# Kernel tuning notes

Measured on AMD Instinct MI355X. Metric: run time of the kernel, lower is better.

Reference implementation:

```python
import jax, jax.numpy as jnp
import numpy as np

B, H, W, C = 32, 56, 56, 512
WS, SHIFT, NH = 7, 3, 16
N = WS * WS
NW = (H // WS) * (W // WS)
HID = 4 * C
EPS = 1e-5


def _np_constants():
    # log-spaced relative coords table (SwinV2 CPB input), pretrained_window_size=[0,0]
    rh = np.arange(-(WS - 1), WS, dtype=np.float32)
    tbl = np.stack(np.meshgrid(rh, rh, indexing='ij'), axis=-1)  # (2*WS-1, 2*WS-1, 2)
    tbl = tbl / (WS - 1) * 8.0
    tbl = np.sign(tbl) * np.log2(np.abs(tbl) + 1.0) / np.log2(8.0)
    coords = np.stack(np.meshgrid(np.arange(WS), np.arange(WS), indexing='ij'))
    cf = coords.reshape(2, -1)
    rc = (cf[:, :, None] - cf[:, None, :]).transpose(1, 2, 0).copy()  # (N,N,2)
    rc[..., 0] += WS - 1
    rc[..., 1] += WS - 1
    rc[..., 0] *= 2 * WS - 1
    rpi = rc.sum(-1)  # (N,N) indices into the (2*WS-1)^2 table
    # shifted-window attention mask
    img = np.zeros((H, W), dtype=np.float32)
    sl = (slice(0, -WS), slice(-WS, -SHIFT), slice(-SHIFT, None))
    cnt = 0
    for hs in sl:
        for ws in sl:
            img[hs, ws] = cnt
            cnt += 1
    mw = img.reshape(H // WS, WS, W // WS, WS).transpose(0, 2, 1, 3).reshape(-1, N)
    am = mw[:, None, :] - mw[:, :, None]
    attn_mask = np.where(am != 0, -100.0, 0.0).astype(np.float32)  # (NW,N,N)
    return tbl.reshape(-1, 2).astype(np.float32), rpi.reshape(-1), attn_mask

TBL_NP, RPI_NP, MASK_NP = _np_constants()


def _ln(x, g, b):
    mu = jnp.mean(x, -1, keepdims=True)
    var = jnp.mean((x - mu) ** 2, -1, keepdims=True)
    return (x - mu) * jax.lax.rsqrt(var + EPS) * g + b


def _win_part(x):  # (B,H,W,C) -> (B*NW, N, C)
    x = x.reshape(B, H // WS, WS, W // WS, WS, C).transpose(0, 1, 3, 2, 4, 5)
    return x.reshape(-1, N, C)


def _win_rev(w):  # (B*NW, N, C) -> (B,H,W,C)
    x = w.reshape(B, H // WS, W // WS, WS, WS, C).transpose(0, 1, 3, 2, 4, 5)
    return x.reshape(B, H, W, C)


def setup_inputs() -> dict:
    key = jax.random.key(0)
    ks = jax.random.split(key, 8)
    s = 0.02
    return {
        'x': jax.random.normal(ks[0], (B, H * W, C), jnp.float32),
        'qkv_w': jax.random.normal(ks[1], (3 * C, C), jnp.float32) * s,
        'q_bias': jnp.zeros((C,), jnp.float32),
        'v_bias': jnp.zeros((C,), jnp.float32),
        'logit_scale': jnp.log(10.0) * jnp.ones((NH, 1, 1), jnp.float32),
        'cpb_w1': jax.random.normal(ks[2], (512, 2), jnp.float32) * s,
        'cpb_b1': jnp.zeros((512,), jnp.float32),
        'cpb_w2': jax.random.normal(ks[3], (NH, 512), jnp.float32) * s,
        'proj_w': jax.random.normal(ks[4], (C, C), jnp.float32) * s,
        'proj_b': jnp.zeros((C,), jnp.float32),
        'norm1_g': jnp.ones((C,), jnp.float32),
        'norm1_b': jnp.zeros((C,), jnp.float32),
        'fc1_w': jax.random.normal(ks[5], (HID, C), jnp.float32) * s,
        'fc1_b': jnp.zeros((HID,), jnp.float32),
        'fc2_w': jax.random.normal(ks[6], (C, HID), jnp.float32) * s,
        'fc2_b': jnp.zeros((C,), jnp.float32),
        'norm2_g': jnp.ones((C,), jnp.float32),
        'norm2_b': jnp.zeros((C,), jnp.float32),
    }


def reference(x, qkv_w, q_bias, v_bias, logit_scale, cpb_w1, cpb_b1, cpb_w2,
              proj_w, proj_b, norm1_g, norm1_b, fc1_w, fc1_b, fc2_w, fc2_b,
              norm2_g, norm2_b):
    tbl = jnp.asarray(TBL_NP)
    mask = jnp.asarray(MASK_NP)
    shortcut = x
    xi = x.reshape(B, H, W, C)
    xi = jnp.roll(xi, shift=(-SHIFT, -SHIFT), axis=(1, 2))
    xw = _win_part(xi)  # (B*NW, N, C)
    qkv_bias = jnp.concatenate([q_bias, jnp.zeros_like(v_bias), v_bias])
    qkv = xw @ qkv_w.T + qkv_bias
    qkv = qkv.reshape(-1, N, 3, NH, C // NH).transpose(2, 0, 3, 1, 4)
    q, k, v = qkv[0], qkv[1], qkv[2]  # (B_, NH, N, hd)
    qn = q / jnp.maximum(jnp.linalg.norm(q, axis=-1, keepdims=True), 1e-12)
    kn = k / jnp.maximum(jnp.linalg.norm(k, axis=-1, keepdims=True), 1e-12)
    scale = jnp.exp(jnp.minimum(logit_scale, jnp.log(100.0)))  # (NH,1,1)
    attn = jnp.einsum('bhnd,bhmd->bhnm', qn, kn) * scale
    # CPB MLP -> relative position bias
    hcb = jax.nn.relu(tbl @ cpb_w1.T + cpb_b1)       # (169, 512)
    bias_tbl = hcb @ cpb_w2.T                        # (169, NH)
    rpb = bias_tbl[RPI_NP].reshape(N, N, NH).transpose(2, 0, 1)
    rpb = 16.0 * jax.nn.sigmoid(rpb)
    attn = attn + rpb[None]
    attn = attn.reshape(B, NW, NH, N, N) + mask[None, :, None]
    attn = jax.nn.softmax(attn.reshape(-1, NH, N, N), axis=-1)
    out = jnp.einsum('bhnm,bhmd->bhnd', attn, v).transpose(0, 2, 1, 3).reshape(-1, N, C)
    out = out @ proj_w.T + proj_b
    xi = _win_rev(out)
    xi = jnp.roll(xi, shift=(SHIFT, SHIFT), axis=(1, 2)).reshape(B, H * W, C)
    x = shortcut + _ln(xi, norm1_g, norm1_b)  # SwinV2 post-norm residual
    hmlp = jax.nn.gelu(x @ fc1_w.T + fc1_b, approximate=False)
    m = hmlp @ fc2_w.T + fc2_b
    x = x + _ln(m, norm2_g, norm2_b)
    return x
```

## Files before the change

### kernel.cpp

```cpp
#include <hip/hip_runtime.h>

typedef unsigned short u16;
typedef unsigned int   u32;

using f32x4  = __attribute__((ext_vector_type(4))) float;
using bf16x8 = __attribute__((ext_vector_type(8))) short;

__device__ __forceinline__ float bf2f(u16 u){
  union { u32 i; float f; } x; x.i = ((u32)u) << 16; return x.f;
}
__device__ __forceinline__ u16 f2bf(float f){
  union { float f; u32 i; } x; x.f = f;
  u32 r = x.i + 0x7FFFu + ((x.i >> 16) & 1u);
  return (u16)(r >> 16);
}
__device__ __forceinline__ float gelu_f(float v){
  float u = 0.7978845608f * v * (1.f + 0.044715f*v*v);
  float e = __expf(2.f*u);
  return 0.5f*v*(2.f - 2.f/(e + 1.f));
}

__device__ __forceinline__ void glds16(const void* g, void* l){
  __builtin_amdgcn_global_load_lds(
      (const __attribute__((address_space(1))) unsigned int*)g,
      (__attribute__((address_space(3))) unsigned int*)(unsigned int)(unsigned long long)l,
      16, 0, 0);
}

__device__ __forceinline__ int rollmap(int m){
  int win = m / 49, n = m % 49;
  int b  = win >> 6, wi = win & 63;
  int wh = wi >> 3, ww = wi & 7;
  int r = n / 7, c = n % 7;
  int sh = wh*7 + r + 3; if (sh >= 56) sh -= 56;
  int sw = ww*7 + c + 3; if (sw >= 56) sw -= 56;
  return b*3136 + sh*56 + sw;
}

template<int EPI, int AMODE>
__global__ __launch_bounds__(256) void gemm_bt(const u16* __restrict__ A,
      const u16* __restrict__ Bw, const float* __restrict__ bias,
      void* __restrict__ outp, int M, int N, int K, int nbn)
{
  __shared__ __align__(16) u16 As[128*32];
  __shared__ __align__(16) u16 Bs[128*32];
  const int t    = threadIdx.x;
  const int lane = t & 63, wave = t >> 6;
  const int wm = wave >> 1, wn = wave & 1;

  const int gl = ((blockIdx.x & 7) * ((int)gridDim.x >> 3)) + (blockIdx.x >> 3);
  const int bm = gl / nbn, bn = gl - bm*nbn;

  const int r0 = t >> 2;
  const int sc = t & 3;
  const int dc = sc ^ ((r0 >> 1) & 3);

  const u16* gB0 = Bw + (size_t)(bn*128 + r0)*K + dc*8;
  const u16* gB1 = gB0 + (size_t)64*K;
  const u16* gA0; const u16* gA1;
  if constexpr (AMODE == 0){
    gA0 = A + (size_t)(bm*128 + r0)*K + dc*8;
    gA1 = gA0 + (size_t)64*K;
  } else {
    gA0 = A + (size_t)rollmap(bm*128 + r0     )*K + dc*8;
    gA1 = A + (size_t)rollmap(bm*128 + r0 + 64)*K + dc*8;
  }

  const int lr = lane & 15, lk = lane >> 4;
  int offA[4], offB[4];
#pragma unroll
  for (int i = 0; i < 4; ++i){
    int ar = wm*64 + i*16 + lr;
    offA[i] = ar*64 + ((lk ^ ((ar >> 1) & 3)) * 16);
    int br = wn*64 + i*16 + lr;
    offB[i] = br*64 + ((lk ^ ((br >> 1) & 3)) * 16);
  }

  f32x4 acc[4][4];
#pragma unroll
  for (int i = 0; i < 4; ++i)
#pragma unroll
    for (int j = 0; j < 4; ++j) acc[i][j] = (f32x4){0.f, 0.f, 0.f, 0.f};

  char* AsB = (char*)As;
  char* BsB = (char*)Bs;

  for (int kt = 0; kt < K; kt += 32){
    __syncthreads();
    glds16(gA0 + kt, AsB +        wave*1024);
    glds16(gA1 + kt, AsB + 4096 + wave*1024);
    glds16(gB0 + kt, BsB +        wave*1024);
    glds16(gB1 + kt, BsB + 4096 + wave*1024);
    __syncthreads();
    bf16x8 fa[4], fb[4];
#pragma unroll
    for (int i = 0; i < 4; ++i){
      fa[i] = *(const bf16x8*)(AsB + offA[i]);
      fb[i] = *(const bf16x8*)(BsB + offB[i]);
    }
#pragma unroll
    for (int i = 0; i < 4; ++i)
#pragma unroll
      for (int j = 0; j < 4; ++j)
        acc[i][j] = __builtin_amdgcn_mfma_f32_16x16x32_bf16(fa[i], fb[j], acc[i][j], 0, 0, 0);
  }

#pragma unroll
  for (int i = 0; i < 4; ++i){
#pragma unroll
    for (int j = 0; j < 4; ++j){
      int cm = bm*128 + wm*64 + i*16 + (lane >> 4)*4;
      int cn = bn*128 + wn*64 + j*16 + (lane & 15);
      float bv = bias[cn];
#pragma unroll
      for (int r = 0; r < 4; ++r){
        float v = acc[i][j][r] + bv;
        if (EPI == 2) v = gelu_f(v);
        if (EPI == 1) ((float*)outp)[(size_t)(cm + r)*N + cn] = v;
        else          ((u16*)  outp)[(size_t)(cm + r)*N + cn] = f2bf(v);
      }
    }
  }
}

__global__ __launch_bounds__(256, 2) void attn_mfma(const u16* __restrict__ qkv,
      const float* __restrict__ rpb, const float* __restrict__ ls,
      u16* __restrict__ outp)
{
  __shared__ __align__(16) u16 Pl[4][64*72];
  __shared__ __align__(16) u16 Vl[4][32*72];
  __shared__ unsigned char regid[64];
  const int tid  = threadIdx.x, lane = tid & 63, wave = tid >> 6;
  const int lc = lane & 15, lg = lane >> 4;
  const int pair = blockIdx.x*4 + wave;
  const int win = pair >> 4, h = pair & 15;

  const u16* qb = qkv + (size_t)win*49*1536 + h*32;
  const u16* kb = qb + 512;
  const u16* vb = qb + 1024;

  if (tid < 49){
    int wi = win & 63, wh = wi >> 3, ww = wi & 7;
    int q7 = (tid*37) >> 8, r7 = tid - q7*7;
    int gh = wh*7 + q7, gw = ww*7 + r7;
    int rh = gh < 49 ? 0 : (gh < 53 ? 1 : 2);
    int rw = gw < 49 ? 0 : (gw < 53 ? 1 : 2);
    regid[tid] = (unsigned char)(rh*3 + rw);
  }

  u16* V = &Vl[wave][0];
#pragma unroll
  for (int it = 0; it < 4; ++it){
    int ch = it*64 + lane;
    int n = ch >> 2, oct = ch & 3;
    union { int4 i4; u16 s[8]; } v8;
    if (n < 49) v8.i4 = *(const int4*)(vb + (size_t)n*1536 + oct*8);
    else        v8.i4 = make_int4(0,0,0,0);
#pragma unroll
    for (int q = 0; q < 8; ++q) V[(oct*8 + q)*72 + n] = v8.s[q];
  }

  const float scale = __expf(fminf(ls[h], 4.6051702f));
  bf16x8 qf[4], kf[4];
#pragma unroll
  for (int ti = 0; ti < 4; ++ti){
    const int n = ti*16 + lc;
    {
      union { int4 i4; u16 s[8]; } raw;
      raw.i4 = *(const int4*)(qb + (size_t)n*1536 + lg*8);
      float f[8]; float ss = 0.f;
#pragma unroll
      for (int q = 0; q < 8; ++q){ f[q] = bf2f(raw.s[q]); ss += f[q]*f[q]; }
      ss += __shfl_xor(ss, 16); ss += __shfl_xor(ss, 32);
      const float inv = scale / fmaxf(sqrtf(ss), 1e-12f);
      union { short s[8]; bf16x8 v; } o;
#pragma unroll
      for (int q = 0; q < 8; ++q) o.s[q] = (short)f2bf(f[q]*inv);
      qf[ti] = o.v;
    }
    {
      union { int4 i4; u16 s[8]; } raw;
      raw.i4 = *(const int4*)(kb + (size_t)n*1536 + lg*8);
      float f[8]; float ss = 0.f;
#pragma unroll
      for (int q = 0; q < 8; ++q){ f[q] = bf2f(raw.s[q]); ss += f[q]*f[q]; }
      ss += __shfl_xor(ss, 16); ss += __shfl_xor(ss, 32);
      const float inv = 1.f / fmaxf(sqrtf(ss), 1e-12f);
      union { short s[8]; bf16x8 v; } o;
#pragma unroll
      for (int q = 0; q < 8; ++q) o.s[q] = (short)f2bf(f[q]*inv);
      kf[ti] = o.v;
    }
  }
  __syncthreads();

  f32x4 acc[4][4];
#pragma unroll
  for (int i = 0; i < 4; ++i)
#pragma unroll
    for (int j = 0; j < 4; ++j) acc[i][j] = (f32x4){0.f,0.f,0.f,0.f};
#pragma unroll
  for (int i = 0; i < 4; ++i)
#pragma unroll
    for (int j = 0; j < 4; ++j)
      acc[i][j] = __builtin_amdgcn_mfma_f32_16x16x32_bf16(qf[i], kf[j], acc[i][j], 0, 0, 0);

  u16* P = &Pl[wave][0];
  int rj[4];
#pragma unroll
  for (int tj = 0; tj < 4; ++tj){
    int j = tj*16 + lc;
    rj[tj] = (int)regid[j < 49 ? j : 0];
  }
  const float* rpbh = rpb + h*2401;
#pragma unroll
  for (int ti = 0; ti < 4; ++ti){
#pragma unroll
    for (int r = 0; r < 4; ++r){
      const int i = ti*16 + lg*4 + r;
      const bool iv = i < 49;
      const int ic = iv ? i : 0;
      const int ri = (int)regid[ic];
      const float* rrow = rpbh + ic*49;
      float sv[4];
#pragma unroll
      for (int tj = 0; tj < 4; ++tj){
        const int j = tj*16 + lc;
        float t2 = acc[ti][tj][r] + rrow[j < 49 ? j : 0];
        if (ri != rj[tj]) t2 -= 100.f;
        sv[tj] = (iv && j < 49) ? t2 : -1e30f;
      }
      float mx = fmaxf(fmaxf(sv[0],sv[1]), fmaxf(sv[2],sv[3]));
      mx = fmaxf(mx, __shfl_xor(mx, 1));
      mx = fmaxf(mx, __shfl_xor(mx, 2));
      mx = fmaxf(mx, __shfl_xor(mx, 4));
      mx = fmaxf(mx, __shfl_xor(mx, 8));
      float p[4], sum = 0.f;
#pragma unroll
      for (int tj = 0; tj < 4; ++tj){ p[tj] = __expf(sv[tj] - mx); sum += p[tj]; }
      sum += __shfl_xor(sum, 1); sum += __shfl_xor(sum, 2);
      sum += __shfl_xor(sum, 4); sum += __shfl_xor(sum, 8);
      const float rs = __builtin_amdgcn_rcpf(sum);
#pragma unroll
      for (int tj = 0; tj < 4; ++tj) P[i*72 + tj*16 + lc] = f2bf(p[tj]*rs);
    }
  }
  __syncthreads();

  f32x4 o[4][2];
#pragma unroll
  for (int i = 0; i < 4; ++i){ o[i][0] = (f32x4){0.f,0.f,0.f,0.f}; o[i][1] = (f32x4){0.f,0.f,0.f,0.f}; }
#pragma unroll
  for (int ks = 0; ks < 2; ++ks){
    bf16x8 pa[4], vf[2];
#pragma unroll
    for (int ti = 0; ti < 4; ++ti)
      pa[ti] = *(const bf16x8*)((const char*)P + (ti*16 + lc)*144 + (ks*4 + lg)*16);
#pragma unroll
    for (int tc = 0; tc < 2; ++tc)
      vf[tc] = *(const bf16x8*)((const char*)V + (tc*16 + lc)*144 + (ks*4 + lg)*16);
#pragma unroll
    for (int ti = 0; ti < 4; ++ti)
#pragma unroll
      for (int tc = 0; tc < 2; ++tc)
        o[ti][tc] = __builtin_amdgcn_mfma_f32_16x16x32_bf16(pa[ti], vf[tc], o[ti][tc], 0, 0, 0);
  }

#pragma unroll
  for (int ti = 0; ti < 4; ++ti){
#pragma unroll
    for (int tc = 0; tc < 2; ++tc){
#pragma unroll
      for (int r = 0; r < 4; ++r){
        const int i = ti*16 + lg*4 + r;
        if (i < 49)
          outp[((size_t)win*49 + i)*512 + h*32 + tc*16 + lc] = f2bf(o[ti][tc][r]);
      }
    }
  }
}

__global__ __launch_bounds__(256) void ln1_kernel(const float* __restrict__ x,
      const u16* __restrict__ y, const float* __restrict__ g, const float* __restrict__ bt,
      float* __restrict__ xout, u16* __restrict__ xbf)
{
  __shared__ float red[8];
  const int t = blockIdx.x;
  const int b = t / 3136, s = t % 3136;
  const int hh = s / 56, ww2 = s % 56;
  int ph = hh + 53; if (ph >= 56) ph -= 56;
  int pw = ww2 + 53; if (pw >= 56) pw -= 56;
  const int win = b*64 + (ph/7)*8 + (pw/7);
  const int n   = (ph%7)*7 + (pw%7);
  const u16* yr = y + ((size_t)win*49 + n)*512;
  const int c = threadIdx.x * 2;
  u32 u = *(const u32*)(yr + c);
  float vx = bf2f((u16)(u & 0xffff)), vy = bf2f((u16)(u >> 16));
  float sum = vx + vy, sq = vx*vx + vy*vy;
#pragma unroll
  for (int off = 32; off; off >>= 1){ sum += __shfl_xor(sum, off); sq += __shfl_xor(sq, off); }
  if ((threadIdx.x & 63) == 0){ red[threadIdx.x >> 6] = sum; red[(threadIdx.x >> 6) + 4] = sq; }
  __syncthreads();
  sum = red[0]+red[1]+red[2]+red[3];
  sq  = red[4]+red[5]+red[6]+red[7];
  const float mu  = sum * (1.f/512.f);
  const float inv = rsqrtf(fmaxf(sq * (1.f/512.f) - mu*mu, 0.f) + 1e-5f);
  const float* xr = x + (size_t)t*512;
  float2 xv = *(const float2*)(xr + c);
  float o0 = xv.x + (vx - mu)*inv*g[c]   + bt[c];
  float o1 = xv.y + (vy - mu)*inv*g[c+1] + bt[c+1];
  float* orow = xout + (size_t)t*512;
  orow[c] = o0; orow[c+1] = o1;
  *(u32*)(xbf + (size_t)t*512 + c) = (u32)f2bf(o0) | ((u32)f2bf(o1) << 16);
}

__global__ __launch_bounds__(256) void ln2_kernel(const u16* __restrict__ m,
      const float* __restrict__ g, const float* __restrict__ bt, float* __restrict__ out)
{
  __shared__ float red[8];
  const int t = blockIdx.x;
  const int c = threadIdx.x * 2;
  u32 u = *(const u32*)(m + (size_t)t*512 + c);
  float v0 = bf2f((u16)(u & 0xffff)), v1 = bf2f((u16)(u >> 16));
  float sum = v0 + v1, sq = v0*v0 + v1*v1;
#pragma unroll
  for (int off = 32; off; off >>= 1){ sum += __shfl_xor(sum, off); sq += __shfl_xor(sq, off); }
  if ((threadIdx.x & 63) == 0){ red[threadIdx.x >> 6] = sum; red[(threadIdx.x >> 6) + 4] = sq; }
  __syncthreads();
  sum = red[0]+red[1]+red[2]+red[3];
  sq  = red[4]+red[5]+red[6]+red[7];
  const float mu  = sum * (1.f/512.f);
  const float inv = rsqrtf(fmaxf(sq * (1.f/512.f) - mu*mu, 0.f) + 1e-5f);
  float* orow = out + (size_t)t*512;
  orow[c]   += (v0 - mu)*inv*g[c]   + bt[c];
  orow[c+1] += (v1 - mu)*inv*g[c+1] + bt[c+1];
}

__global__ void cast_bf16_kernel(const float* __restrict__ in, u16* __restrict__ out, int n4){
  int i = blockIdx.x*256 + threadIdx.x;
  if (i >= n4) return;
  float4 v = *(const float4*)(in + (size_t)i*4);
  u32 lo = (u32)f2bf(v.x) | ((u32)f2bf(v.y) << 16);
  u32 hi = (u32)f2bf(v.z) | ((u32)f2bf(v.w) << 16);
  *(uint2*)(out + (size_t)i*4) = make_uint2(lo, hi);
}
__global__ void qkvbias_kernel(const float* __restrict__ qb, const float* __restrict__ vb,
                               float* __restrict__ out){
  int i = blockIdx.x*256 + threadIdx.x;
  if (i >= 1536) return;
  out[i] = i < 512 ? qb[i] : (i < 1024 ? 0.f : vb[i - 1024]);
}
__device__ __forceinline__ float cpb_coord(int d){
  float v = (float)(d - 6) * (8.f/6.f);
  float m = log2f(fabsf(v) + 1.f) * (1.f/3.f);
  return v > 0.f ? m : (v < 0.f ? -m : 0.f);
}
__global__ void cpb_kernel(const float* __restrict__ w1, const float* __restrict__ b1,
                           const float* __restrict__ w2, float* __restrict__ btbl){
  int idx = blockIdx.x*256 + threadIdx.x;
  if (idx >= 169*16) return;
  int e = idx >> 4, h = idx & 15;
  float t0 = cpb_coord(e / 13), t1 = cpb_coord(e % 13);
  float acc = 0.f;
  for (int jj = 0; jj < 512; ++jj){
    float hid = fmaxf(t0*w1[jj*2] + t1*w1[jj*2+1] + b1[jj], 0.f);
    acc += hid * w2[h*512 + jj];
  }
  btbl[e*16 + h] = acc;
}
__global__ void rpb_kernel(const float* __restrict__ btbl, float* __restrict__ rpb){
  int idx = blockIdx.x*256 + threadIdx.x;
  if (idx >= 16*49*49) return;
  int hh = idx / 2401, ij = idx % 2401, i = ij / 49, j = ij % 49;
  int dr = i/7 - j/7 + 6, dc = i%7 - j%7 + 6;
  float bb = btbl[(dr*13 + dc)*16 + hh];
  rpb[idx] = 16.f / (1.f + __expf(-bb));
}

extern "C" void kernel_launch(void* const* d_in, const int* in_sizes, int n_in,
                              void* d_out, int out_size, void* d_ws, size_t ws_size,
                              hipStream_t stream)
{
  const float* x    = (const float*)d_in[0];
  const float* qkvw = (const float*)d_in[1];
  const float* qb   = (const float*)d_in[2];
  const float* vb   = (const float*)d_in[3];
  const float* ls   = (const float*)d_in[4];
  const float* cw1  = (const float*)d_in[5];
  const float* cb1  = (const float*)d_in[6];
  const float* cw2  = (const float*)d_in[7];
  const float* pw   = (const float*)d_in[8];
  const float* pb   = (const float*)d_in[9];
  const float* n1g  = (const float*)d_in[10];
  const float* n1b  = (const float*)d_in[11];
  const float* f1w  = (const float*)d_in[12];
  const float* f1b  = (const float*)d_in[13];
  const float* f2w  = (const float*)d_in[14];
  const float* f2b  = (const float*)d_in[15];
  const float* n2g  = (const float*)d_in[16];
  const float* n2b  = (const float*)d_in[17];

  char* ws = (char*)d_ws;
  const size_t SZ_BIG = (size_t)100352 * 2048 * 2;
  const size_t SZ_MID = (size_t)100352 * 512  * 2;
  size_t o = SZ_BIG + SZ_MID;
  u16* wqkv  = (u16*)(ws + o); o += (size_t)1536*512*2;
  u16* wproj = (u16*)(ws + o); o += (size_t)512*512*2;
  u16* wfc1  = (u16*)(ws + o); o += (size_t)2048*512*2;
  u16* wfc2  = (u16*)(ws + o); o += (size_t)512*2048*2;
  float* qkvbias = (float*)(ws + o); o += 1536*4;
  float* btbl    = (float*)(ws + o); o += 2704*4;
  float* rpb     = (float*)(ws + o); o += 38416*4;

  u16*   xbf   = (u16*)ws;
  u16*   qkvo  = (u16*)(ws + (size_t)100352*512*2);
  u16*   y_h   = (u16*)ws;
  u16*   big_h = (u16*)ws;
  u16*   mid   = (u16*)(ws + SZ_BIG);
  float* out   = (float*)d_out;

  cast_bf16_kernel<<<768,  256, 0, stream>>>(qkvw, wqkv, 1536*512/4);
  cast_bf16_kernel<<<256,  256, 0, stream>>>(pw,  wproj, 512*512/4);
  cast_bf16_kernel<<<1024, 256, 0, stream>>>(f1w, wfc1, 2048*512/4);
  cast_bf16_kernel<<<1024, 256, 0, stream>>>(f2w, wfc2, 512*2048/4);
  qkvbias_kernel<<<6, 256, 0, stream>>>(qb, vb, qkvbias);
  cpb_kernel<<<11, 256, 0, stream>>>(cw1, cb1, cw2, btbl);
  rpb_kernel<<<151, 256, 0, stream>>>(btbl, rpb);
  cast_bf16_kernel<<<50176, 256, 0, stream>>>(x, xbf, 100352*512/4);

  gemm_bt<0,2><<<784*12, 256, 0, stream>>>(xbf, wqkv, qkvbias,
                                           (void*)qkvo, 100352, 1536, 512, 12);
  attn_mfma<<<8192, 256, 0, stream>>>(qkvo, rpb, ls, mid);
  gemm_bt<0,0><<<784*4, 256, 0, stream>>>(mid, wproj, pb,
                                          (void*)y_h, 100352, 512, 512, 4);
  ln1_kernel<<<100352, 256, 0, stream>>>(x, y_h, n1g, n1b, out, mid);
  gemm_bt<2,0><<<784*16, 256, 0, stream>>>(mid, wfc1, f1b,
                                           (void*)big_h, 100352, 2048, 512, 16);
  gemm_bt<0,0><<<784*4, 256, 0, stream>>>(big_h, wfc2, f2b,
                                          (void*)mid, 100352, 512, 2048, 4);
  ln2_kernel<<<100352, 256, 0, stream>>>(mid, n2g, n2b, out);
}
```

Baseline: 1.617 ms.

## Triple-buffer LDS in GEMM with async global-to-LDS prefetch two tiles ahead

Replaces the single-buffered A/B LDS tiles with a three-stage ring buffer. Global-to-LDS loads for tile k+2 are issued before computing tile k, and a fine-grained vmcnt wait plus one barrier per iteration replaces the two __syncthreads. This is meant to hide global load latency behind MFMA work and cut barrier stalls. It raises LDS use to 48KB per block, which can lower occupancy.

```diff
diff --git a/kernel.cpp b/kernel.cpp
--- a/kernel.cpp
+++ b/kernel.cpp
@@ -42,8 +42,7 @@
       const u16* __restrict__ Bw, const float* __restrict__ bias,
       void* __restrict__ outp, int M, int N, int K, int nbn)
 {
-  __shared__ __align__(16) u16 As[128*32];
-  __shared__ __align__(16) u16 Bs[128*32];
+  __shared__ __align__(16) char LDS[3*16384];
   const int t    = threadIdx.x;
   const int lane = t & 63, wave = t >> 6;
   const int wm = wave >> 1, wn = wave & 1;
@@ -82,28 +81,50 @@
 #pragma unroll
     for (int j = 0; j < 4; ++j) acc[i][j] = (f32x4){0.f, 0.f, 0.f, 0.f};
 
-  char* AsB = (char*)As;
-  char* BsB = (char*)Bs;
-
-  for (int kt = 0; kt < K; kt += 32){
-    __syncthreads();
-    glds16(gA0 + kt, AsB +        wave*1024);
-    glds16(gA1 + kt, AsB + 4096 + wave*1024);
-    glds16(gB0 + kt, BsB +        wave*1024);
-    glds16(gB1 + kt, BsB + 4096 + wave*1024);
-    __syncthreads();
+  auto STAGE = [&](int kt, int buf){
+    char* Ld = LDS + buf*16384;
+    glds16(gA0 + kt, Ld +         wave*1024);
+    glds16(gA1 + kt, Ld +  4096 + wave*1024);
+    glds16(gB0 + kt, Ld +  8192 + wave*1024);
+    glds16(gB1 + kt, Ld + 12288 + wave*1024);
+  };
+  auto COMPUTE = [&](int buf){
+    const char* Ld = LDS + buf*16384;
     bf16x8 fa[4], fb[4];
 #pragma unroll
     for (int i = 0; i < 4; ++i){
-      fa[i] = *(const bf16x8*)(AsB + offA[i]);
-      fb[i] = *(const bf16x8*)(BsB + offB[i]);
+      fa[i] = *(const bf16x8*)(Ld + offA[i]);
+      fb[i] = *(const bf16x8*)(Ld + 8192 + offB[i]);
     }
 #pragma unroll
     for (int i = 0; i < 4; ++i)
 #pragma unroll
       for (int j = 0; j < 4; ++j)
         acc[i][j] = __builtin_amdgcn_mfma_f32_16x16x32_bf16(fa[i], fb[j], acc[i][j], 0, 0, 0);
-  }
+  };
+
+  const int NT = K >> 5;
+  STAGE(0, 0);
+  STAGE(32, 1);
+  asm volatile("s_waitcnt vmcnt(4)" ::: "memory");
+  __builtin_amdgcn_s_barrier();
+  asm volatile("" ::: "memory");
+  int cur = 0;
+  for (int t2 = 0; t2 + 2 < NT; ++t2){
+    int nx2 = cur + 2; if (nx2 >= 3) nx2 -= 3;
+    STAGE((t2 + 2) << 5, nx2);
+    COMPUTE(cur);
+    asm volatile("s_waitcnt vmcnt(4) lgkmcnt(0)" ::: "memory");
+    __builtin_amdgcn_s_barrier();
+    asm volatile("" ::: "memory");
+    ++cur; if (cur == 3) cur = 0;
+  }
+  COMPUTE(cur);
+  asm volatile("s_waitcnt vmcnt(0) lgkmcnt(0)" ::: "memory");
+  __builtin_amdgcn_s_barrier();
+  asm volatile("" ::: "memory");
+  ++cur; if (cur == 3) cur = 0;
+  COMPUTE(cur);
 
 #pragma unroll
   for (int i = 0; i < 4; ++i){
```

Measured after the change: 1.502 ms. -7.1%, faster.
